# Performance work log

Hardware: AMD Instinct MI355X
Metric: run time of the kernel (lower is better)

## Reference

```python
import jax, jax.numpy as jnp
import numpy as np

N_NODES = 100000
N_EDGES = 600000
IN_FEAT = 128
OUT_FEAT = 128
REL_NUM = 5


def setup_inputs() -> dict:
    key = jax.random.key(0)
    k = jax.random.split(key, 7)
    h = jax.random.normal(k[0], (N_NODES, IN_FEAT), dtype=jnp.float32)
    weight = jax.random.normal(k[1], (REL_NUM, IN_FEAT, OUT_FEAT), dtype=jnp.float32)
    W_0 = jax.random.normal(k[2], (IN_FEAT, OUT_FEAT), dtype=jnp.float32)
    norm = jax.random.uniform(k[3], (N_EDGES,), dtype=jnp.float32)
    src = jax.random.randint(k[4], (N_EDGES,), 0, N_NODES, dtype=jnp.int32)
    dst = jax.random.randint(k[5], (N_EDGES,), 0, N_NODES, dtype=jnp.int32)
    edge_id = jax.random.randint(k[6], (N_EDGES,), 0, REL_NUM, dtype=jnp.int32)
    return {"h": h, "weight": weight, "W_0": W_0, "norm": norm,
            "src": src, "dst": dst, "edge_id": edge_id}


def reference(h, weight, W_0, norm, src, dst, edge_id):
    # Per-edge msg = h[src] @ weight[edge_id] * norm.
    # Equivalent, efficient form: transform all nodes by every relation weight
    # once (R is small), then gather per edge instead of materializing an
    # [E, in, out] weight tensor.
    all_h = jnp.einsum('ni,rio->rno', h, weight)          # [R, N, out]
    msg = all_h[edge_id, src] * norm[:, None]             # [E, out]
    h_sum = jax.ops.segment_sum(msg, dst, num_segments=h.shape[0])  # [N, out]
    out = jax.nn.relu(h @ W_0 + h_sum)                    # [N, out]
    return out
```

## Files before the change

kernel.cpp:

```cpp
#include <hip/hip_runtime.h>
#include <hip/hip_bf16.h>


#define NN   100000
#define NE   600000
#define FEAT 128
#define RNUM 5
#define KTOT 768
#define CAP  32

#define SCAT_B 2344
#define PREP_T (NN * 32 + FEAT * KTOT)
#define PREP_B ((PREP_T + 255) / 256)

typedef __attribute__((ext_vector_type(8))) short short8;
typedef __attribute__((ext_vector_type(4))) float float4v;

static __device__ __forceinline__ unsigned short f2bf(float x) {
  union { float f; unsigned u; } v; v.f = x;
  unsigned r = v.u + 0x7FFFu + ((v.u >> 16) & 1u);
  return (unsigned short)(r >> 16);
}

__global__ void k_prep(const int* __restrict__ src, const int* __restrict__ dst,
                       const int* __restrict__ eid, const float* __restrict__ norm,
                       const float* __restrict__ h, const float* __restrict__ weight,
                       const float* __restrict__ W0, int* __restrict__ cnt,
                       int2* __restrict__ s_edge, unsigned short* __restrict__ hb,
                       unsigned short* __restrict__ Bt) {
  int bid = blockIdx.x;
  if (bid < SCAT_B) {
    int e = bid * 256 + threadIdx.x;
    if (e < NE) {
      int d = dst[e];
      int p = atomicAdd(&cnt[d], 1);
      if (p < CAP) {
        union { float f; int i; } nb; nb.f = norm[e];
        s_edge[(size_t)d * CAP + p] = make_int2(src[e] | (eid[e] << 20), nb.i);
      }
    }
  } else {
    int t = (bid - SCAT_B) * 256 + threadIdx.x;
    if (t < NN * 32) {
      float4v v = *(const float4v*)(h + (size_t)t * 4);
      unsigned long long p = (unsigned long long)f2bf(v[0])
                           | ((unsigned long long)f2bf(v[1]) << 16)
                           | ((unsigned long long)f2bf(v[2]) << 32)
                           | ((unsigned long long)f2bf(v[3]) << 48);
      *(unsigned long long*)(hb + (size_t)t * 4) = p;
    } else {
      int u = t - NN * 32;
      if (u < FEAT * KTOT) {
        int j = u & 7, g = u >> 3;
        int ln = g & 63, n0 = (g >> 6) & 7, c = g >> 9;
        int o = n0 * 16 + (ln & 15);
        int k = c * 32 + ((ln >> 4) << 3) + j;
        float v = (k < 640) ? weight[(k >> 7) * 16384 + (k & 127) * 128 + o]
                            : W0[(k - 640) * 128 + o];
        Bt[u] = f2bf(v);
      }
    }
  }
}

static __device__ __forceinline__ void accum_edge(float acc[RNUM][8], int2 e,
                                                  uint4 v) {
  union { int i; float f; } nb; nb.i = e.y;
  int r = e.x >> 20;
  float nm[RNUM];
#pragma unroll
  for (int rr = 0; rr < RNUM; ++rr) nm[rr] = (r == rr) ? nb.f : 0.f;
  float f[8];
  unsigned w[4] = {v.x, v.y, v.z, v.w};
#pragma unroll
  for (int d = 0; d < 4; ++d) {
    union { unsigned u; float g; } lo, hi;
    lo.u = w[d] << 16; hi.u = w[d] & 0xFFFF0000u;
    f[2 * d] = lo.g; f[2 * d + 1] = hi.g;
  }
#pragma unroll
  for (int rr = 0; rr < RNUM; ++rr)
#pragma unroll
    for (int i = 0; i < 8; ++i) acc[rr][i] += nm[rr] * f[i];
}

__global__ __launch_bounds__(256, 2) void k_fused(
    const unsigned short* __restrict__ hb, const int* __restrict__ cnt,
    const int2* __restrict__ s_edge, const unsigned short* __restrict__ Bt,
    float* __restrict__ out) {
  __shared__ uint4 Atile[4 * 1280];
  int tid = threadIdx.x;
  int wv = tid >> 6, lane = tid & 63;
  int blockbase = blockIdx.x * 64;
  int nodebase = blockbase + wv * 16;
  int g = lane >> 4, t = lane & 15;
  const uint4* hb4 = (const uint4*)hb;

#pragma unroll 1
  for (int b = 0; b < 4; ++b) {
    int node = nodebase + b * 4 + g;
    int glen = 0;
    if (node < NN) {
      glen = cnt[node];
      if (glen > CAP) glen = CAP;
    } else node = NN - 1;
    const int2* ep = s_edge + (size_t)node * CAP;
    float acc[RNUM][8] = {};
    int j = 0;
    for (; j + 2 <= glen; j += 2) {
      int2 e0 = ep[j], e1 = ep[j + 1];
      uint4 v0 = hb4[(e0.x & 0xFFFFF) * 16 + t];
      uint4 v1 = hb4[(e1.x & 0xFFFFF) * 16 + t];
      accum_edge(acc, e0, v0);
      accum_edge(acc, e1, v1);
    }
    if (j < glen) {
      int2 e = ep[j];
      uint4 v = hb4[(e.x & 0xFFFFF) * 16 + t];
      accum_edge(acc, e, v);
    }
    int row = b * 4 + g;
#pragma unroll
    for (int rr = 0; rr < RNUM; ++rr) {
      uint4 pk;
      pk.x = (unsigned)f2bf(acc[rr][0]) | ((unsigned)f2bf(acc[rr][1]) << 16);
      pk.y = (unsigned)f2bf(acc[rr][2]) | ((unsigned)f2bf(acc[rr][3]) << 16);
      pk.z = (unsigned)f2bf(acc[rr][4]) | ((unsigned)f2bf(acc[rr][5]) << 16);
      pk.w = (unsigned)f2bf(acc[rr][6]) | ((unsigned)f2bf(acc[rr][7]) << 16);
      Atile[wv * 1280 + (rr * 4 + (t >> 2)) * 64 + (t & 3) * 16 + row] = pk;
    }
  }
  __syncthreads();

  int m = lane & 15, q = lane >> 4;
  float4v cacc[4][2];
#pragma unroll
  for (int tt = 0; tt < 4; ++tt)
#pragma unroll
    for (int u = 0; u < 2; ++u) cacc[tt][u] = (float4v){0.f, 0.f, 0.f, 0.f};

  const unsigned short* Hp[4];
#pragma unroll
  for (int tt = 0; tt < 4; ++tt) {
    int ar = blockbase + tt * 16 + m;
    if (ar >= NN) ar = NN - 1;
    Hp[tt] = hb + (size_t)ar * FEAT + q * 8;
  }

  for (int c = 0; c < 24; ++c) {
    short8 bf0 = *(const short8*)&Bt[((c * 8 + 2 * wv) * 64 + lane) * 8];
    short8 bf1 = *(const short8*)&Bt[((c * 8 + 2 * wv + 1) * 64 + lane) * 8];
#pragma unroll
    for (int tt = 0; tt < 4; ++tt) {
      short8 af;
      if (c < 20) af = *(const short8*)&Atile[tt * 1280 + c * 64 + lane];
      else        af = *(const short8*)(Hp[tt] + (c - 20) * 32);
      cacc[tt][0] = __builtin_amdgcn_mfma_f32_16x16x32_bf16(af, bf0, cacc[tt][0], 0, 0, 0);
      cacc[tt][1] = __builtin_amdgcn_mfma_f32_16x16x32_bf16(af, bf1, cacc[tt][1], 0, 0, 0);
    }
  }
#pragma unroll
  for (int tt = 0; tt < 4; ++tt) {
#pragma unroll
    for (int u = 0; u < 2; ++u) {
#pragma unroll
      for (int r = 0; r < 4; ++r) {
        int row = blockbase + tt * 16 + q * 4 + r;
        if (row < NN) {
          float v = cacc[tt][u][r];
          out[(size_t)row * FEAT + (2 * wv + u) * 16 + m] = v > 0.f ? v : 0.f;
        }
      }
    }
  }
}

__global__ void k_slow_mm(const float* __restrict__ h, const float* __restrict__ W0,
                          float* __restrict__ out) {
  __shared__ float hn[128];
  int n = blockIdx.x, t = threadIdx.x;
  hn[t] = h[(size_t)n * 128 + t];
  __syncthreads();
  float a = 0.f;
  for (int i = 0; i < 128; ++i) a += hn[i] * W0[i * 128 + t];
  out[(size_t)n * 128 + t] = a;
}
__global__ void k_slow_edge(const float* __restrict__ h, const float* __restrict__ weight,
                            const float* __restrict__ norm, const int* __restrict__ src,
                            const int* __restrict__ dst, const int* __restrict__ eid,
                            float* __restrict__ out) {
  __shared__ float hs[128];
  int e = blockIdx.x, t = threadIdx.x;
  hs[t] = h[(size_t)src[e] * 128 + t];
  __syncthreads();
  const float* W = weight + (size_t)eid[e] * 16384;
  float a = 0.f;
  for (int i = 0; i < 128; ++i) a += hs[i] * W[i * 128 + t];
  atomicAdd(&out[(size_t)dst[e] * 128 + t], a * norm[e]);
}
__global__ void k_slow_relu(float* out) {
  int i = blockIdx.x * 256 + threadIdx.x;
  if (i < NN * FEAT) out[i] = fmaxf(out[i], 0.f);
}

extern "C" void kernel_launch(void* const* d_in, const int* in_sizes, int n_in,
                              void* d_out, int out_size, void* d_ws, size_t ws_size,
                              hipStream_t stream) {
  const float* h      = (const float*)d_in[0];
  const float* weight = (const float*)d_in[1];
  const float* W0     = (const float*)d_in[2];
  const float* norm   = (const float*)d_in[3];
  const int*   src    = (const int*)d_in[4];
  const int*   dst    = (const int*)d_in[5];
  const int*   eid    = (const int*)d_in[6];
  float* out = (float*)d_out;

  char* ws = (char*)d_ws;
  size_t off = 0;
  auto wsalloc = [&](size_t bytes) -> char* {
    char* p = ws + off;
    off += (bytes + 255) & ~(size_t)255;
    return p;
  };
  unsigned short* hb  = (unsigned short*)wsalloc((size_t)NN * FEAT * 2);
  unsigned short* Bt  = (unsigned short*)wsalloc((size_t)FEAT * KTOT * 2);
  int*   cnt      = (int*)wsalloc((size_t)NN * 4);
  int2*  s_edge   = (int2*)wsalloc((size_t)NN * CAP * 8 + 256);

  if (ws_size >= off) {
    hipMemsetAsync(cnt, 0, (size_t)NN * 4, stream);
    k_prep <<<SCAT_B + PREP_B, 256, 0, stream>>>(src, dst, eid, norm, h, weight,
                                                 W0, cnt, s_edge, hb, Bt);
    k_fused<<<(NN + 63) / 64, 256, 0, stream>>>(hb, cnt, s_edge, Bt, out);
  } else {
    k_slow_mm  <<<NN, 128, 0, stream>>>(h, W0, out);
    k_slow_edge<<<NE, 128, 0, stream>>>(h, weight, norm, src, dst, eid, out);
    k_slow_relu<<<(NN * FEAT + 255) / 256, 256, 0, stream>>>(out);
  }
}
```

Baseline: 249.8 us.

## Restructure fused kernel into 32-node blocks of 512 threads with swizzled LDS tile

Each 512-thread block now handles 32 nodes, and each wave aggregates only 4 nodes, with no sequential 4-iteration loop. The self-feature rows are staged into LDS alongside the aggregated relation features, and an XOR swizzle is applied to avoid bank conflicts. In the MFMA phase each of 8 waves computes one 16-column output slice for two 16-row tiles. This raises occupancy and parallelism for the latency-bound gather and shrinks per-wave register state. In exchange, each block reloads all B fragments for fewer rows, and bounds checks are dropped, relying on NN being divisible by 32.

```diff
diff --git a/kernel.cpp b/kernel.cpp
--- a/kernel.cpp
+++ b/kernel.cpp
@@ -6,11 +6,11 @@
 #define NE   600000
 #define FEAT 128
 #define RNUM 5
-#define KTOT 768
 #define CAP  32
+#define KC   24
 
 #define SCAT_B 2344
-#define PREP_T (NN * 32 + FEAT * KTOT)
+#define PREP_T (NN * 32 + FEAT * KC * 32)
 #define PREP_B ((PREP_T + 255) / 256)
 
 typedef __attribute__((ext_vector_type(8))) short short8;
@@ -50,7 +50,7 @@
       *(unsigned long long*)(hb + (size_t)t * 4) = p;
     } else {
       int u = t - NN * 32;
-      if (u < FEAT * KTOT) {
+      if (u < FEAT * KC * 32) {
         int j = u & 7, g = u >> 3;
         int ln = g & 63, n0 = (g >> 6) & 7, c = g >> 9;
         int o = n0 * 16 + (ln & 15);
@@ -84,93 +84,73 @@
     for (int i = 0; i < 8; ++i) acc[rr][i] += nm[rr] * f[i];
 }
 
-__global__ __launch_bounds__(256, 2) void k_fused(
+__global__ __launch_bounds__(512, 6) void k_fused(
     const unsigned short* __restrict__ hb, const int* __restrict__ cnt,
     const int2* __restrict__ s_edge, const unsigned short* __restrict__ Bt,
     float* __restrict__ out) {
-  __shared__ uint4 Atile[4 * 1280];
+  __shared__ uint4 Atile[2 * KC * 64];
   int tid = threadIdx.x;
   int wv = tid >> 6, lane = tid & 63;
-  int blockbase = blockIdx.x * 64;
-  int nodebase = blockbase + wv * 16;
   int g = lane >> 4, t = lane & 15;
+  int base = blockIdx.x * 32;
+  int node = base + wv * 4 + g;
+  int row = (wv & 3) * 4 + g;
+  uint4* Aw = Atile + (wv >> 2) * (KC * 64);
   const uint4* hb4 = (const uint4*)hb;
 
-#pragma unroll 1
-  for (int b = 0; b < 4; ++b) {
-    int node = nodebase + b * 4 + g;
-    int glen = 0;
-    if (node < NN) {
-      glen = cnt[node];
-      if (glen > CAP) glen = CAP;
-    } else node = NN - 1;
-    const int2* ep = s_edge + (size_t)node * CAP;
-    float acc[RNUM][8] = {};
-    int j = 0;
-    for (; j + 2 <= glen; j += 2) {
-      int2 e0 = ep[j], e1 = ep[j + 1];
-      uint4 v0 = hb4[(e0.x & 0xFFFFF) * 16 + t];
-      uint4 v1 = hb4[(e1.x & 0xFFFFF) * 16 + t];
-      accum_edge(acc, e0, v0);
-      accum_edge(acc, e1, v1);
-    }
-    if (j < glen) {
-      int2 e = ep[j];
-      uint4 v = hb4[(e.x & 0xFFFFF) * 16 + t];
-      accum_edge(acc, e, v);
-    }
-    int row = b * 4 + g;
-#pragma unroll
-    for (int rr = 0; rr < RNUM; ++rr) {
-      uint4 pk;
-      pk.x = (unsigned)f2bf(acc[rr][0]) | ((unsigned)f2bf(acc[rr][1]) << 16);
-      pk.y = (unsigned)f2bf(acc[rr][2]) | ((unsigned)f2bf(acc[rr][3]) << 16);
-      pk.z = (unsigned)f2bf(acc[rr][4]) | ((unsigned)f2bf(acc[rr][5]) << 16);
-      pk.w = (unsigned)f2bf(acc[rr][6]) | ((unsigned)f2bf(acc[rr][7]) << 16);
-      Atile[wv * 1280 + (rr * 4 + (t >> 2)) * 64 + (t & 3) * 16 + row] = pk;
-    }
+  int glen = cnt[node]; if (glen > CAP) glen = CAP;
+  const int2* ep = s_edge + (size_t)node * CAP;
+  float acc[RNUM][8] = {};
+  int j = 0;
+  for (; j + 2 <= glen; j += 2) {
+    int2 e0 = ep[j], e1 = ep[j + 1];
+    uint4 v0 = hb4[(e0.x & 0xFFFFF) * 16 + t];
+    uint4 v1 = hb4[(e1.x & 0xFFFFF) * 16 + t];
+    accum_edge(acc, e0, v0);
+    accum_edge(acc, e1, v1);
+  }
+  if (j < glen) {
+    int2 e = ep[j];
+    uint4 v = hb4[(e.x & 0xFFFFF) * 16 + t];
+    accum_edge(acc, e, v);
+  }
+  int q = t & 3, cb = t >> 2;
+#pragma unroll
+  for (int rr = 0; rr < RNUM; ++rr) {
+    int c = rr * 4 + cb;
+    uint4 pk;
+    pk.x = (unsigned)f2bf(acc[rr][0]) | ((unsigned)f2bf(acc[rr][1]) << 16);
+    pk.y = (unsigned)f2bf(acc[rr][2]) | ((unsigned)f2bf(acc[rr][3]) << 16);
+    pk.z = (unsigned)f2bf(acc[rr][4]) | ((unsigned)f2bf(acc[rr][5]) << 16);
+    pk.w = (unsigned)f2bf(acc[rr][6]) | ((unsigned)f2bf(acc[rr][7]) << 16);
+    Aw[c * 64 + q * 16 + (row ^ ((c * 4 + q) & 7))] = pk;
+  }
+  {
+    int c = 20 + cb;
+    Aw[c * 64 + q * 16 + (row ^ ((c * 4 + q) & 7))] = hb4[(size_t)node * 16 + t];
   }
   __syncthreads();
 
-  int m = lane & 15, q = lane >> 4;
-  float4v cacc[4][2];
-#pragma unroll
-  for (int tt = 0; tt < 4; ++tt)
-#pragma unroll
-    for (int u = 0; u < 2; ++u) cacc[tt][u] = (float4v){0.f, 0.f, 0.f, 0.f};
-
-  const unsigned short* Hp[4];
-#pragma unroll
-  for (int tt = 0; tt < 4; ++tt) {
-    int ar = blockbase + tt * 16 + m;
-    if (ar >= NN) ar = NN - 1;
-    Hp[tt] = hb + (size_t)ar * FEAT + q * 8;
-  }
-
-  for (int c = 0; c < 24; ++c) {
-    short8 bf0 = *(const short8*)&Bt[((c * 8 + 2 * wv) * 64 + lane) * 8];
-    short8 bf1 = *(const short8*)&Bt[((c * 8 + 2 * wv + 1) * 64 + lane) * 8];
-#pragma unroll
-    for (int tt = 0; tt < 4; ++tt) {
-      short8 af;
-      if (c < 20) af = *(const short8*)&Atile[tt * 1280 + c * 64 + lane];
-      else        af = *(const short8*)(Hp[tt] + (c - 20) * 32);
-      cacc[tt][0] = __builtin_amdgcn_mfma_f32_16x16x32_bf16(af, bf0, cacc[tt][0], 0, 0, 0);
-      cacc[tt][1] = __builtin_amdgcn_mfma_f32_16x16x32_bf16(af, bf1, cacc[tt][1], 0, 0, 0);
-    }
-  }
-#pragma unroll
-  for (int tt = 0; tt < 4; ++tt) {
-#pragma unroll
-    for (int u = 0; u < 2; ++u) {
-#pragma unroll
-      for (int r = 0; r < 4; ++r) {
-        int row = blockbase + tt * 16 + q * 4 + r;
-        if (row < NN) {
-          float v = cacc[tt][u][r];
-          out[(size_t)row * FEAT + (2 * wv + u) * 16 + m] = v > 0.f ? v : 0.f;
-        }
-      }
+  int m = lane & 15, qq = lane >> 4;
+  float4v cacc[2];
+  cacc[0] = (float4v){0.f, 0.f, 0.f, 0.f};
+  cacc[1] = (float4v){0.f, 0.f, 0.f, 0.f};
+#pragma unroll
+  for (int c = 0; c < KC; ++c) {
+    int sx = qq * 16 + (m ^ ((c * 4 + qq) & 7));
+    short8 af0 = *(const short8*)&Atile[c * 64 + sx];
+    short8 af1 = *(const short8*)&Atile[KC * 64 + c * 64 + sx];
+    short8 bf  = *(const short8*)&Bt[((c * 8 + wv) * 64 + lane) * 8];
+    cacc[0] = __builtin_amdgcn_mfma_f32_16x16x32_bf16(af0, bf, cacc[0], 0, 0, 0);
+    cacc[1] = __builtin_amdgcn_mfma_f32_16x16x32_bf16(af1, bf, cacc[1], 0, 0, 0);
+  }
+#pragma unroll
+  for (int tt = 0; tt < 2; ++tt) {
+#pragma unroll
+    for (int r = 0; r < 4; ++r) {
+      int rrow = base + tt * 16 + qq * 4 + r;
+      float v = cacc[tt][r];
+      out[(size_t)rrow * FEAT + wv * 16 + m] = v > 0.f ? v : 0.f;
     }
   }
 }
@@ -223,7 +203,7 @@
     return p;
   };
   unsigned short* hb  = (unsigned short*)wsalloc((size_t)NN * FEAT * 2);
-  unsigned short* Bt  = (unsigned short*)wsalloc((size_t)FEAT * KTOT * 2);
+  unsigned short* Bt  = (unsigned short*)wsalloc((size_t)FEAT * KC * 32 * 2);
   int*   cnt      = (int*)wsalloc((size_t)NN * 4);
   int2*  s_edge   = (int2*)wsalloc((size_t)NN * CAP * 8 + 256);
 
@@ -231,7 +211,7 @@
     hipMemsetAsync(cnt, 0, (size_t)NN * 4, stream);
     k_prep <<<SCAT_B + PREP_B, 256, 0, stream>>>(src, dst, eid, norm, h, weight,
                                                  W0, cnt, s_edge, hb, Bt);
-    k_fused<<<(NN + 63) / 64, 256, 0, stream>>>(hb, cnt, s_edge, Bt, out);
+    k_fused<<<NN / 32, 512, 0, stream>>>(hb, cnt, s_edge, Bt, out);
   } else {
     k_slow_mm  <<<NN, 128, 0, stream>>>(h, W0, out);
     k_slow_edge<<<NE, 128, 0, stream>>>(h, weight, norm, src, dst, eid, out);
```

Result: faster. 203.3 us (-18.6%).
